# Performance work log

Hardware: AMD Instinct MI355X
Metric: run time of the kernel (lower is better)

## Reference

```python
import jax, jax.numpy as jnp
from jax import lax
import numpy as np

W_SSIM = 0.5
W_SMOOTH = 0.1
W_LR = 1.0
C1 = 0.01 ** 2
C2 = 0.03 ** 2


def avg3(x):
    # 3x3 stride-1 VALID average pool (matches F.avg_pool2d(x, 3, 1))
    return lax.reduce_window(x, 0.0, lax.add, (1, 1, 3, 3), (1, 1, 1, 1), 'VALID') / 9.0


def resize_ac(img, oh, ow):
    # bilinear resize with align_corners=True, separable gathers
    B, C, H, W = img.shape
    ys = jnp.linspace(0.0, H - 1.0, oh)
    xs = jnp.linspace(0.0, W - 1.0, ow)
    y0 = jnp.floor(ys).astype(jnp.int32); y1 = jnp.minimum(y0 + 1, H - 1); wy = ys - y0
    x0 = jnp.floor(xs).astype(jnp.int32); x1 = jnp.minimum(x0 + 1, W - 1); wx = xs - x0
    r = img[:, :, y0, :] * (1.0 - wy)[None, None, :, None] + img[:, :, y1, :] * wy[None, None, :, None]
    return r[:, :, :, x0] * (1.0 - wx) + r[:, :, :, x1] * wx


def warp_h(img, disp, sign):
    # horizontal bilinear warp: sample img at x + sign*disp (disp in units of image width),
    # align_corners=True pixel mapping, zeros padding outside the image.
    B, C, H, W = img.shape
    xb = jnp.linspace(0.0, 1.0, W)
    px = (xb[None, None, :] + sign * disp[:, 0, :, :]) * (W - 1)  # [B,H,W] pixel coords
    x0 = jnp.floor(px); f = px - x0
    x0i = x0.astype(jnp.int32); x1i = x0i + 1
    v0 = ((x0i >= 0) & (x0i < W)).astype(img.dtype)
    v1 = ((x1i >= 0) & (x1i < W)).astype(img.dtype)
    i0 = jnp.broadcast_to(jnp.clip(x0i, 0, W - 1)[:, None], (B, C, H, W))
    i1 = jnp.broadcast_to(jnp.clip(x1i, 0, W - 1)[:, None], (B, C, H, W))
    g0 = jnp.take_along_axis(img, i0, axis=3)
    g1 = jnp.take_along_axis(img, i1, axis=3)
    return g0 * (v0 * (1.0 - f))[:, None] + g1 * (v1 * f)[:, None]


def ssim(x, y):
    mu_x = avg3(x); mu_y = avg3(y)
    sig_x = avg3(x * x) - mu_x ** 2
    sig_y = avg3(y * y) - mu_y ** 2
    sig_xy = avg3(x * y) - mu_x * mu_y
    s = ((2 * mu_x * mu_y + C1) * (2 * sig_xy + C2)) / ((mu_x ** 2 + mu_y ** 2 + C1) * (sig_x + sig_y + C2))
    return jnp.clip((1.0 - s) / 2.0, 0.0, 1.0)


def smoothness(disp, img):
    dgx = disp[:, :, :, :-1] - disp[:, :, :, 1:]
    dgy = disp[:, :, :-1, :] - disp[:, :, 1:, :]
    igx = img[:, :, :, :-1] - img[:, :, :, 1:]
    igy = img[:, :, :-1, :] - img[:, :, 1:, :]
    wx = jnp.exp(-jnp.mean(jnp.abs(igx), axis=1, keepdims=True))
    wy = jnp.exp(-jnp.mean(jnp.abs(igy), axis=1, keepdims=True))
    return jnp.mean(jnp.abs(dgx * wx)) + jnp.mean(jnp.abs(dgy * wy))


def compute_loss(disps, left, right):
    B, _, H, W = left.shape
    img_loss = 0.0
    lr_loss = 0.0
    sm_loss = 0.0
    for i, d in enumerate(disps):
        r = 2 ** i
        h, w = H // r, W // r
        lpy = left if i == 0 else resize_ac(left, h, w)
        rpy = right if i == 0 else resize_ac(right, h, w)
        dl = d[:, 0:1]; dr = d[:, 1:2]
        left_est = warp_h(rpy, dl, -1.0)
        right_est = warp_h(lpy, dr, 1.0)
        rl_disp = warp_h(dr, dl, -1.0)
        lr_disp = warp_h(dl, dr, 1.0)
        l1_l = jnp.mean(jnp.abs(left_est - lpy))
        l1_r = jnp.mean(jnp.abs(right_est - rpy))
        ss_l = jnp.mean(ssim(left_est, lpy))
        ss_r = jnp.mean(ssim(right_est, rpy))
        img_loss = img_loss + W_SSIM * ss_l + (1 - W_SSIM) * l1_l + W_SSIM * ss_r + (1 - W_SSIM) * l1_r
        lr_loss = lr_loss + jnp.mean(jnp.abs(rl_disp - dl)) + jnp.mean(jnp.abs(lr_disp - dr))
        sm_loss = sm_loss + (smoothness(dl, lpy) + smoothness(dr, rpy)) / r
    return img_loss + W_SMOOTH * sm_loss + W_LR * lr_loss


def setup_inputs() -> dict:
    key = jax.random.key(0)
    ks = jax.random.split(key, 6)
    B, H, W = 16, 384, 768
    inp = {}
    for i in range(4):
        r = 2 ** i
        # disparities in units of image width; scaled to realistic ~[0, 0.1]
        inp[f'disp{i}'] = jax.random.uniform(ks[i], (B, 2, H // r, W // r), dtype=jnp.float32) * 0.1
    inp['left_image'] = jax.random.uniform(ks[4], (B, 3, H, W), dtype=jnp.float32)
    inp['right_image'] = jax.random.uniform(ks[5], (B, 3, H, W), dtype=jnp.float32)
    return inp


def reference(disp0, disp1, disp2, disp3, left_image, right_image):
    return compute_loss([disp0, disp1, disp2, disp3], left_image, right_image)
```

## Files before the change

kernel.cpp:

```cpp
#include <hip/hip_runtime.h>
#include <math.h>

#define C1F 1.0e-4f
#define C2F 9.0e-4f
#define TX 32
#define TY 8


struct ScaleArgs {
    const float* disp;
    const float* lp;
    const float* rp;
    int h, w, nx, ny, blk0, accoff;
};

__device__ __forceinline__ float2 f2(float v) { return make_float2(v, v); }
__device__ __forceinline__ float2 f2abs(float2 a) {
    return make_float2(fabsf(a.x), fabsf(a.y));
}

__device__ __forceinline__ void warp_coeffs(float px, int W, int& i0, int& i1,
                                            float& w0, float& w1) {
    float x0f = floorf(px);
    float f = px - x0f;
    int x0i = (int)x0f;
    int x1i = x0i + 1;
    float v0 = (x0i >= 0 && x0i < W) ? 1.f : 0.f;
    float v1 = (x1i >= 0 && x1i < W) ? 1.f : 0.f;
    i0 = min(max(x0i, 0), W - 1);
    i1 = min(max(x1i, 0), W - 1);
    w0 = v0 * (1.f - f);
    w1 = v1 * f;
}

template<int N>
__device__ __forceinline__ void block_acc(const float* vals, float* gacc) {
    __shared__ float sacc[N];
    if (threadIdx.x < N) sacc[threadIdx.x] = 0.f;
    __syncthreads();
#pragma unroll
    for (int k = 0; k < N; ++k) {
        float v = vals[k];
#pragma unroll
        for (int off = 32; off > 0; off >>= 1) v += __shfl_down(v, off, 64);
        if ((threadIdx.x & 63) == 0) atomicAdd(&sacc[k], v);
    }
    __syncthreads();
    if (threadIdx.x < N) atomicAdd(&gacc[threadIdx.x], sacc[threadIdx.x]);
}

__global__ void k_zero(float* acc) {
    if (threadIdx.x < 64) acc[threadIdx.x] = 0.f;
}

__device__ __forceinline__ void fused_tile(const ScaleArgs& sa, int t,
                                           float* __restrict__ accbase) {
    __shared__ float4 simg[3][(TY + 2) * (TX + 2)];
    __shared__ float2 sdisp[(TY + 2) * (TX + 2)];

    const int h = sa.h, w = sa.w;
    float* acc = accbase + sa.accoff;

    const int tileX = t % sa.nx;
    int t2 = t / sa.nx;
    const int tileY = t2 % sa.ny;
    const int b = t2 / sa.ny;

    const int xo0 = tileX * TX;
    const int yo0 = tileY * TY;
    const int tid = threadIdx.x;
    const float Wm1 = (float)(w - 1);
    const float invWm1 = 1.f / Wm1;
    const int chs = h * w;

    const float* __restrict__ dl_base = sa.disp + (b * 2 + 0) * chs;
    const float* __restrict__ dr_base = sa.disp + (b * 2 + 1) * chs;
    const float* __restrict__ limg = sa.lp + b * 3 * chs;
    const float* __restrict__ rimg = sa.rp + b * 3 * chs;

    const int NS = (TY + 2) * (TX + 2);
    const int nk = (tid + 256 < NS) ? 2 : 1;
    int xs[2], ys[2];
    float dlv[2], drv[2];
#pragma unroll
    for (int k = 0; k < 2; ++k) {
        if (k < nk) {
            int i = tid + k * 256;
            int sx = i % (TX + 2);
            int sy = i / (TX + 2);
            int x = min(max(xo0 - 1 + sx, 0), w - 1);
            int y = min(max(yo0 - 1 + sy, 0), h - 1);
            xs[k] = x; ys[k] = y;
            int off = y * w + x;
            dlv[k] = dl_base[off];
            drv[k] = dr_base[off];
        }
    }
    int i0L[2], i1L[2], i0R[2], i1R[2];
    float w0L[2], w1L[2], w0R[2], w1R[2];
    float lvv[2][3], rvv[2][3], gr0[2][3], gr1[2][3], gl0[2][3], gl1[2][3];
#pragma unroll
    for (int k = 0; k < 2; ++k) {
        if (k < nk) {
            float xb = (float)xs[k] * invWm1;
            warp_coeffs((xb - dlv[k]) * Wm1, w, i0L[k], i1L[k], w0L[k], w1L[k]);
            warp_coeffs((xb + drv[k]) * Wm1, w, i0R[k], i1R[k], w0R[k], w1R[k]);
            int rowoff = ys[k] * w;
#pragma unroll
            for (int c = 0; c < 3; ++c) {
                int co = c * chs + rowoff;
                lvv[k][c] = limg[co + xs[k]];
                rvv[k][c] = rimg[co + xs[k]];
                gr0[k][c] = rimg[co + i0L[k]];
                gr1[k][c] = rimg[co + i1L[k]];
                gl0[k][c] = limg[co + i0R[k]];
                gl1[k][c] = limg[co + i1R[k]];
            }
        }
    }
#pragma unroll
    for (int k = 0; k < 2; ++k) {
        if (k < nk) {
            int i = tid + k * 256;
            sdisp[i] = make_float2(dlv[k], drv[k]);
#pragma unroll
            for (int c = 0; c < 3; ++c) {
                float le = gr0[k][c] * w0L[k] + gr1[k][c] * w1L[k];
                float re = gl0[k][c] * w0R[k] + gl1[k][c] * w1R[k];
                simg[c][i] = make_float4(le, re, lvv[k][c], rvv[k][c]);
            }
        }
    }
    __syncthreads();

    float sums[8] = {0.f, 0.f, 0.f, 0.f, 0.f, 0.f, 0.f, 0.f};
    const int tx = tid % TX, ty = tid / TX;
    const int x = xo0 + tx, y = yo0 + ty;
    if (x < w && y < h) {
        const int s = (ty + 1) * (TX + 2) + (tx + 1);
        float2 dd = sdisp[s];
        float dl = dd.x, dr = dd.y;
#pragma unroll
        for (int c = 0; c < 3; ++c) {
            float4 v = simg[c][s];
            float2 d = f2abs(make_float2(v.x, v.y) - make_float2(v.z, v.w));
            sums[0] += d.x;
            sums[1] += d.y;
        }
        {
            float xb = (float)x * invWm1;
            int i0, i1; float w0, w1;
            warp_coeffs((xb - dl) * Wm1, w, i0, i1, w0, w1);
            const float* dr_row = dr_base + y * w;
            float rl = dr_row[i0] * w0 + dr_row[i1] * w1;
            sums[2] += fabsf(rl - dl);
            warp_coeffs((xb + dr) * Wm1, w, i0, i1, w0, w1);
            const float* dl_row = dl_base + y * w;
            float lr = dl_row[i0] * w0 + dl_row[i1] * w1;
            sums[3] += fabsf(lr - dr);
        }
        const float third = 1.f / 3.f;
        if (x < w - 1) {
            float2 d1 = sdisp[s + 1];
            float2 alr = f2(0.f);
#pragma unroll
            for (int c = 0; c < 3; ++c) {
                float4 v = simg[c][s];
                float4 v1 = simg[c][s + 1];
                alr = alr + f2abs(make_float2(v.z, v.w) - make_float2(v1.z, v1.w));
            }
            sums[4] += fabsf((dl - d1.x) * __expf(-alr.x * third)) +
                       fabsf((dr - d1.y) * __expf(-alr.y * third));
        }
        if (y < h - 1) {
            float2 d1 = sdisp[s + (TX + 2)];
            float2 alr = f2(0.f);
#pragma unroll
            for (int c = 0; c < 3; ++c) {
                float4 v = simg[c][s];
                float4 v1 = simg[c][s + (TX + 2)];
                alr = alr + f2abs(make_float2(v.z, v.w) - make_float2(v1.z, v1.w));
            }
            sums[5] += fabsf((dl - d1.x) * __expf(-alr.x * third)) +
                       fabsf((dr - d1.y) * __expf(-alr.y * third));
        }
        if (x >= 1 && x <= w - 2 && y >= 1 && y <= h - 2) {
            const float2 inv9 = f2(1.f / 9.f);
            const float2 c1 = f2(C1F), c2 = f2(C2F);
            const float2 two = f2(2.f), one = f2(1.f), half_ = f2(0.5f);
#pragma unroll 1
            for (int c = 0; c < 3; ++c) {
                float2 sX = f2(0.f), sY = f2(0.f);
                float2 sXX = f2(0.f), sYY = f2(0.f), sXY = f2(0.f);
#pragma unroll
                for (int dy = 0; dy < 3; ++dy) {
#pragma unroll
                    for (int dx = 0; dx < 3; ++dx) {
                        float4 v = simg[c][(ty + dy) * (TX + 2) + (tx + dx)];
                        float2 a = make_float2(v.x, v.y);
                        float2 bb = make_float2(v.z, v.w);
                        sX = sX + a;
                        sY = sY + bb;
                        sXX = sXX + a * a;
                        sYY = sYY + bb * bb;
                        sXY = sXY + a * bb;
                    }
                }
                float2 mx = sX * inv9, my = sY * inv9;
                float2 vx = sXX * inv9 - mx * mx;
                float2 vy = sYY * inv9 - my * my;
                float2 vxy = sXY * inv9 - mx * my;
                float2 num = (two * mx * my + c1) * (two * vxy + c2);
                float2 den = (mx * mx + my * my + c1) * (vx + vy + c2);
                float2 ss = make_float2(num.x * __builtin_amdgcn_rcpf(den.x),
                                        num.y * __builtin_amdgcn_rcpf(den.y));
                float2 v = (one - ss) * half_;
                sums[6] += fminf(fmaxf(v.x, 0.f), 1.f);
                sums[7] += fminf(fmaxf(v.y, 0.f), 1.f);
            }
        }
    }
    block_acc<8>(sums, acc);
}

__global__ void __launch_bounds__(256, 4)
k_fused0_resize(ScaleArgs s0, float* __restrict__ accbase,
                const float* __restrict__ left, const float* __restrict__ right,
                float* __restrict__ lo1, float* __restrict__ ro1,
                float* __restrict__ lo2, float* __restrict__ ro2,
                float* __restrict__ lo3, float* __restrict__ ro3,
                int B, int H, int W,
                int nFusedBlocks, long long n1, long long n2, long long n3) {
    if ((int)blockIdx.x < nFusedBlocks) {
        fused_tile(s0, blockIdx.x, accbase);
        return;
    }
    long long idx = (long long)(blockIdx.x - nFusedBlocks) * blockDim.x + threadIdx.x;
    int oh, ow;
    float* lo;
    float* ro;
    if (idx < n1) {
        oh = H / 2; ow = W / 2; lo = lo1; ro = ro1;
    } else if (idx < n1 + n2) {
        idx -= n1; oh = H / 4; ow = W / 4; lo = lo2; ro = ro2;
    } else if (idx < n1 + n2 + n3) {
        idx -= n1 + n2; oh = H / 8; ow = W / 8; lo = lo3; ro = ro3;
    } else {
        return;
    }
    long long half = (long long)B * 3 * oh * ow;
    const float* src = left;
    float* dst = lo;
    if (idx >= half) { src = right; dst = ro; idx -= half; }
    int x = (int)(idx % ow);
    long long t = idx / ow;
    int y = (int)(t % oh);
    t /= oh;
    int c = (int)(t % 3);
    int b = (int)(t / 3);
    float sy = (float)(H - 1) / (float)(oh - 1);
    float sx = (float)(W - 1) / (float)(ow - 1);
    float fy = y * sy;
    float fx = x * sx;
    int y0 = (int)floorf(fy); float wy = fy - (float)y0;
    int x0 = (int)floorf(fx); float wx = fx - (float)x0;
    int y1 = min(y0 + 1, H - 1); y0 = min(y0, H - 1);
    int x1 = min(x0 + 1, W - 1); x0 = min(x0, W - 1);
    const float* p = src + ((long long)b * 3 + c) * H * W;
    float a00 = p[(long long)y0 * W + x0];
    float a10 = p[(long long)y1 * W + x0];
    float a01 = p[(long long)y0 * W + x1];
    float a11 = p[(long long)y1 * W + x1];
    float r0 = a00 * (1.f - wy) + a10 * wy;
    float r1 = a01 * (1.f - wy) + a11 * wy;
    dst[(((long long)b * 3 + c) * oh + y) * ow + x] = r0 * (1.f - wx) + r1 * wx;
}

__global__ void __launch_bounds__(256, 4)
k_fused_small(ScaleArgs s1, ScaleArgs s2, ScaleArgs s3,
              float* __restrict__ accbase) {
    ScaleArgs sa;
    {
        int blk = blockIdx.x;
        if (blk >= s3.blk0)      sa = s3;
        else if (blk >= s2.blk0) sa = s2;
        else                     sa = s1;
    }
    fused_tile(sa, blockIdx.x - sa.blk0, accbase);
}

__global__ void k_final(const float* __restrict__ acc, float* __restrict__ out,
                        int B, int H, int W) {
    if (threadIdx.x != 0 || blockIdx.x != 0) return;
    float img = 0.f, lr = 0.f, sm = 0.f;
    for (int i = 0; i < 4; ++i) {
        int r = 1 << i;
        int h = H / r, w = W / r;
        const float* a = acc + i * 8;
        float Nl1 = (float)B * 3.f * (float)h * (float)w;
        float Nss = (float)B * 3.f * (float)(h - 2) * (float)(w - 2);
        float Nlr = (float)B * (float)h * (float)w;
        float Nsx = (float)B * (float)h * (float)(w - 1);
        float Nsy = (float)B * (float)(h - 1) * (float)w;
        img += 0.5f * (a[6] / Nss) + 0.5f * (a[0] / Nl1)
             + 0.5f * (a[7] / Nss) + 0.5f * (a[1] / Nl1);
        lr += a[2] / Nlr + a[3] / Nlr;
        sm += (a[4] / Nsx + a[5] / Nsy) / (float)r;
    }
    out[0] = img + 0.1f * sm + 1.0f * lr;
}

extern "C" void kernel_launch(void* const* d_in, const int* in_sizes, int n_in,
                              void* d_out, int out_size, void* d_ws, size_t ws_size,
                              hipStream_t stream) {
    const int B = 16, H = 384, W = 768;
    const float* disp[4] = {(const float*)d_in[0], (const float*)d_in[1],
                            (const float*)d_in[2], (const float*)d_in[3]};
    const float* left = (const float*)d_in[4];
    const float* right = (const float*)d_in[5];
    float* out = (float*)d_out;

    float* acc = (float*)d_ws;
    float* pyr = acc + 256;
    long long sz1 = (long long)B * 3 * (H / 2) * (W / 2);
    long long sz2 = (long long)B * 3 * (H / 4) * (W / 4);
    long long sz3 = (long long)B * 3 * (H / 8) * (W / 8);
    float* lp1 = pyr;
    float* rp1 = lp1 + sz1;
    float* lp2 = rp1 + sz1;
    float* rp2 = lp2 + sz2;
    float* lp3 = rp2 + sz2;
    float* rp3 = lp3 + sz3;

    const int TB = 256;
    const float* lp[4] = {left, lp1, lp2, lp3};
    const float* rp[4] = {right, rp1, rp2, rp3};
    ScaleArgs sa[4];
    for (int i = 0; i < 4; ++i) {
        int r = 1 << i;
        int h = H / r, w = W / r;
        sa[i].disp = disp[i];
        sa[i].lp = lp[i];
        sa[i].rp = rp[i];
        sa[i].h = h;
        sa[i].w = w;
        sa[i].nx = w / TX;
        sa[i].ny = h / TY;
        sa[i].accoff = i * 8;
        sa[i].blk0 = 0;
    }

    hipLaunchKernelGGL(k_zero, dim3(1), dim3(64), 0, stream, acc);

    {
        int nFused = sa[0].nx * sa[0].ny * B;
        long long n1 = 2 * sz1, n2 = 2 * sz2, n3 = 2 * sz3;
        long long nrElem = n1 + n2 + n3;
        int nResize = (int)((nrElem + TB - 1) / TB);
        hipLaunchKernelGGL(k_fused0_resize, dim3((unsigned)(nFused + nResize)), dim3(TB), 0, stream,
                           sa[0], acc, left, right, lp1, rp1, lp2, rp2, lp3, rp3,
                           B, H, W, nFused, n1, n2, n3);
    }

    {
        int b1 = sa[1].nx * sa[1].ny * B;
        int b2 = sa[2].nx * sa[2].ny * B;
        int b3 = sa[3].nx * sa[3].ny * B;
        sa[1].blk0 = 0;
        sa[2].blk0 = b1;
        sa[3].blk0 = b1 + b2;
        hipLaunchKernelGGL(k_fused_small, dim3((unsigned)(b1 + b2 + b3)), dim3(TB), 0, stream,
                           sa[1], sa[2], sa[3], acc);
    }
    hipLaunchKernelGGL(k_final, dim3(1), dim3(64), 0, stream, acc, out, B, H, W);
}
```

Before: 505.4 us.

## Fuse pyramid resize into small-scale tiles and merge all scales into one kernel

Removes the materialized image pyramid. Each small-scale tile now computes the bilinear-resized pixels, including the warped gathers, on the fly from the full-resolution images. All four scales run in a single launch, with XCD-aware block swizzling and a last-block ticket counter that does the final reduction in place of a separate kernel. This saves the pyramid write and read-back plus two launches, at the cost of more arithmetic and scattered full-resolution gathers in the small-scale tiles.

```diff
diff --git a/kernel.cpp b/kernel.cpp
--- a/kernel.cpp
+++ b/kernel.cpp
@@ -5,13 +5,16 @@
 #define C2F 9.0e-4f
 #define TX 32
 #define TY 8
+#define NSTAGE ((TY + 2) * (TX + 2))
 
 
 struct ScaleArgs {
     const float* disp;
     const float* lp;
     const float* rp;
-    int h, w, nx, ny, blk0, accoff;
+    int h, w, nx, ny, blk0, accoff, ntiles;
+    int Wf, Hf;
+    float syf, sxf;
 };
 
 __device__ __forceinline__ float2 f2(float v) { return make_float2(v, v); }
@@ -49,15 +52,22 @@
     if (threadIdx.x < N) atomicAdd(&gacc[threadIdx.x], sacc[threadIdx.x]);
 }
 
+__device__ __forceinline__ int xcd_swz(int orig, int n) {
+    int q = n >> 3, r = n & 7;
+    int x = orig & 7;
+    int base = (x < r) ? x * (q + 1) : r * (q + 1) + (x - r) * q;
+    return base + (orig >> 3);
+}
+
 __global__ void k_zero(float* acc) {
-    if (threadIdx.x < 64) acc[threadIdx.x] = 0.f;
-}
-
+    acc[threadIdx.x] = 0.f;
+}
+
+template<bool RS>
 __device__ __forceinline__ void fused_tile(const ScaleArgs& sa, int t,
-                                           float* __restrict__ accbase) {
-    __shared__ float4 simg[3][(TY + 2) * (TX + 2)];
-    __shared__ float2 sdisp[(TY + 2) * (TX + 2)];
-
+                                           float* __restrict__ accbase,
+                                           float4 (*__restrict__ simg)[NSTAGE],
+                                           float2* __restrict__ sdisp) {
     const int h = sa.h, w = sa.w;
     float* acc = accbase + sa.accoff;
 
@@ -75,59 +85,120 @@
 
     const float* __restrict__ dl_base = sa.disp + (b * 2 + 0) * chs;
     const float* __restrict__ dr_base = sa.disp + (b * 2 + 1) * chs;
-    const float* __restrict__ limg = sa.lp + b * 3 * chs;
-    const float* __restrict__ rimg = sa.rp + b * 3 * chs;
-
-    const int NS = (TY + 2) * (TX + 2);
-    const int nk = (tid + 256 < NS) ? 2 : 1;
-    int xs[2], ys[2];
-    float dlv[2], drv[2];
-#pragma unroll
-    for (int k = 0; k < 2; ++k) {
-        if (k < nk) {
-            int i = tid + k * 256;
+
+    const int nk = (tid + 256 < NSTAGE) ? 2 : 1;
+
+    if (!RS) {
+        const float* __restrict__ limg = sa.lp + b * 3 * chs;
+        const float* __restrict__ rimg = sa.rp + b * 3 * chs;
+        int xs[2], ys[2];
+        float dlv[2], drv[2];
+#pragma unroll
+        for (int k = 0; k < 2; ++k) {
+            if (k < nk) {
+                int i = tid + k * 256;
+                int sx = i % (TX + 2);
+                int sy = i / (TX + 2);
+                int x = min(max(xo0 - 1 + sx, 0), w - 1);
+                int y = min(max(yo0 - 1 + sy, 0), h - 1);
+                xs[k] = x; ys[k] = y;
+                int off = y * w + x;
+                dlv[k] = dl_base[off];
+                drv[k] = dr_base[off];
+            }
+        }
+        int i0L[2], i1L[2], i0R[2], i1R[2];
+        float w0L[2], w1L[2], w0R[2], w1R[2];
+        float lvv[2][3], rvv[2][3], gr0[2][3], gr1[2][3], gl0[2][3], gl1[2][3];
+#pragma unroll
+        for (int k = 0; k < 2; ++k) {
+            if (k < nk) {
+                float xb = (float)xs[k] * invWm1;
+                warp_coeffs((xb - dlv[k]) * Wm1, w, i0L[k], i1L[k], w0L[k], w1L[k]);
+                warp_coeffs((xb + drv[k]) * Wm1, w, i0R[k], i1R[k], w0R[k], w1R[k]);
+                int rowoff = ys[k] * w;
+#pragma unroll
+                for (int c = 0; c < 3; ++c) {
+                    int co = c * chs + rowoff;
+                    lvv[k][c] = limg[co + xs[k]];
+                    rvv[k][c] = rimg[co + xs[k]];
+                    gr0[k][c] = rimg[co + i0L[k]];
+                    gr1[k][c] = rimg[co + i1L[k]];
+                    gl0[k][c] = limg[co + i0R[k]];
+                    gl1[k][c] = limg[co + i1R[k]];
+                }
+            }
+        }
+#pragma unroll
+        for (int k = 0; k < 2; ++k) {
+            if (k < nk) {
+                int i = tid + k * 256;
+                sdisp[i] = make_float2(dlv[k], drv[k]);
+#pragma unroll
+                for (int c = 0; c < 3; ++c) {
+                    float le = gr0[k][c] * w0L[k] + gr1[k][c] * w1L[k];
+                    float re = gl0[k][c] * w0R[k] + gl1[k][c] * w1R[k];
+                    simg[c][i] = make_float4(le, re, lvv[k][c], rvv[k][c]);
+                }
+            }
+        }
+    } else {
+        const int Wf = sa.Wf;
+        const int chsF = sa.Hf * Wf;
+        const float* __restrict__ limgF = sa.lp + b * 3 * chsF;
+        const float* __restrict__ rimgF = sa.rp + b * 3 * chsF;
+        for (int k = 0; k < nk; ++k) {
+            int i = tid + (k << 8);
             int sx = i % (TX + 2);
             int sy = i / (TX + 2);
             int x = min(max(xo0 - 1 + sx, 0), w - 1);
             int y = min(max(yo0 - 1 + sy, 0), h - 1);
-            xs[k] = x; ys[k] = y;
             int off = y * w + x;
-            dlv[k] = dl_base[off];
-            drv[k] = dr_base[off];
-        }
-    }
-    int i0L[2], i1L[2], i0R[2], i1R[2];
-    float w0L[2], w1L[2], w0R[2], w1R[2];
-    float lvv[2][3], rvv[2][3], gr0[2][3], gr1[2][3], gl0[2][3], gl1[2][3];
-#pragma unroll
-    for (int k = 0; k < 2; ++k) {
-        if (k < nk) {
-            float xb = (float)xs[k] * invWm1;
-            warp_coeffs((xb - dlv[k]) * Wm1, w, i0L[k], i1L[k], w0L[k], w1L[k]);
-            warp_coeffs((xb + drv[k]) * Wm1, w, i0R[k], i1R[k], w0R[k], w1R[k]);
-            int rowoff = ys[k] * w;
+            float dlv = dl_base[off];
+            float drv = dr_base[off];
+            float fy = (float)y * sa.syf;
+            int y0 = (int)floorf(fy);
+            float wy = fy - (float)y0;
+            int y1 = min(y0 + 1, sa.Hf - 1);
+            y0 = min(y0, sa.Hf - 1);
+            float omwy = 1.f - wy;
+            int ro0 = y0 * Wf, ro1 = y1 * Wf;
+            float xb = (float)x * invWm1;
+            int i0L, i1L, i0R, i1R;
+            float w0L, w1L, w0R, w1R;
+            warp_coeffs((xb - dlv) * Wm1, w, i0L, i1L, w0L, w1L);
+            warp_coeffs((xb + drv) * Wm1, w, i0R, i1R, w0R, w1R);
+            int px_[5] = {x, i0L, i1L, i0R, i1R};
+            int x0p[5], x1p[5];
+            float wxp[5];
+#pragma unroll
+            for (int p = 0; p < 5; ++p) {
+                float fx = (float)px_[p] * sa.sxf;
+                int x0 = (int)floorf(fx);
+                wxp[p] = fx - (float)x0;
+                x1p[p] = min(x0 + 1, Wf - 1);
+                x0p[p] = min(x0, Wf - 1);
+            }
+            auto BIL = [&](const float* P0, const float* P1, int p) -> float {
+                float r0 = P0[x0p[p]] * omwy + P1[x0p[p]] * wy;
+                float r1 = P0[x1p[p]] * omwy + P1[x1p[p]] * wy;
+                return r0 * (1.f - wxp[p]) + r1 * wxp[p];
+            };
+            sdisp[i] = make_float2(dlv, drv);
 #pragma unroll
             for (int c = 0; c < 3; ++c) {
-                int co = c * chs + rowoff;
-                lvv[k][c] = limg[co + xs[k]];
-                rvv[k][c] = rimg[co + xs[k]];
-                gr0[k][c] = rimg[co + i0L[k]];
-                gr1[k][c] = rimg[co + i1L[k]];
-                gl0[k][c] = limg[co + i0R[k]];
-                gl1[k][c] = limg[co + i1R[k]];
-            }
-        }
-    }
-#pragma unroll
-    for (int k = 0; k < 2; ++k) {
-        if (k < nk) {
-            int i = tid + k * 256;
-            sdisp[i] = make_float2(dlv[k], drv[k]);
-#pragma unroll
-            for (int c = 0; c < 3; ++c) {
-                float le = gr0[k][c] * w0L[k] + gr1[k][c] * w1L[k];
-                float re = gl0[k][c] * w0R[k] + gl1[k][c] * w1R[k];
-                simg[c][i] = make_float4(le, re, lvv[k][c], rvv[k][c]);
+                const float* L0 = limgF + c * chsF + ro0;
+                const float* L1 = limgF + c * chsF + ro1;
+                const float* R0 = rimgF + c * chsF + ro0;
+                const float* R1 = rimgF + c * chsF + ro1;
+                float lv = BIL(L0, L1, 0);
+                float rv = BIL(R0, R1, 0);
+                float g0 = BIL(R0, R1, 1);
+                float g1 = BIL(R0, R1, 2);
+                float h0 = BIL(L0, L1, 3);
+                float h1 = BIL(L0, L1, 4);
+                simg[c][i] = make_float4(g0 * w0L + g1 * w1L,
+                                         h0 * w0R + h1 * w1R, lv, rv);
             }
         }
     }
@@ -224,90 +295,53 @@
 }
 
 __global__ void __launch_bounds__(256, 4)
-k_fused0_resize(ScaleArgs s0, float* __restrict__ accbase,
-                const float* __restrict__ left, const float* __restrict__ right,
-                float* __restrict__ lo1, float* __restrict__ ro1,
-                float* __restrict__ lo2, float* __restrict__ ro2,
-                float* __restrict__ lo3, float* __restrict__ ro3,
-                int B, int H, int W,
-                int nFusedBlocks, long long n1, long long n2, long long n3) {
-    if ((int)blockIdx.x < nFusedBlocks) {
-        fused_tile(s0, blockIdx.x, accbase);
-        return;
-    }
-    long long idx = (long long)(blockIdx.x - nFusedBlocks) * blockDim.x + threadIdx.x;
-    int oh, ow;
-    float* lo;
-    float* ro;
-    if (idx < n1) {
-        oh = H / 2; ow = W / 2; lo = lo1; ro = ro1;
-    } else if (idx < n1 + n2) {
-        idx -= n1; oh = H / 4; ow = W / 4; lo = lo2; ro = ro2;
-    } else if (idx < n1 + n2 + n3) {
-        idx -= n1 + n2; oh = H / 8; ow = W / 8; lo = lo3; ro = ro3;
+k_main(ScaleArgs s0, ScaleArgs s1, ScaleArgs s2, ScaleArgs s3,
+       float* __restrict__ accbase, float* __restrict__ out,
+       int nTotal, int B, int H, int W) {
+    __shared__ float4 simg[3][NSTAGE];
+    __shared__ float2 sdisp[NSTAGE];
+
+    int blk = blockIdx.x;
+    if (blk < s1.blk0) {
+        int t = xcd_swz(blk, s0.ntiles);
+        fused_tile<false>(s0, t, accbase, simg, sdisp);
     } else {
-        return;
-    }
-    long long half = (long long)B * 3 * oh * ow;
-    const float* src = left;
-    float* dst = lo;
-    if (idx >= half) { src = right; dst = ro; idx -= half; }
-    int x = (int)(idx % ow);
-    long long t = idx / ow;
-    int y = (int)(t % oh);
-    t /= oh;
-    int c = (int)(t % 3);
-    int b = (int)(t / 3);
-    float sy = (float)(H - 1) / (float)(oh - 1);
-    float sx = (float)(W - 1) / (float)(ow - 1);
-    float fy = y * sy;
-    float fx = x * sx;
-    int y0 = (int)floorf(fy); float wy = fy - (float)y0;
-    int x0 = (int)floorf(fx); float wx = fx - (float)x0;
-    int y1 = min(y0 + 1, H - 1); y0 = min(y0, H - 1);
-    int x1 = min(x0 + 1, W - 1); x0 = min(x0, W - 1);
-    const float* p = src + ((long long)b * 3 + c) * H * W;
-    float a00 = p[(long long)y0 * W + x0];
-    float a10 = p[(long long)y1 * W + x0];
-    float a01 = p[(long long)y0 * W + x1];
-    float a11 = p[(long long)y1 * W + x1];
-    float r0 = a00 * (1.f - wy) + a10 * wy;
-    float r1 = a01 * (1.f - wy) + a11 * wy;
-    dst[(((long long)b * 3 + c) * oh + y) * ow + x] = r0 * (1.f - wx) + r1 * wx;
-}
-
-__global__ void __launch_bounds__(256, 4)
-k_fused_small(ScaleArgs s1, ScaleArgs s2, ScaleArgs s3,
-              float* __restrict__ accbase) {
-    ScaleArgs sa;
-    {
-        int blk = blockIdx.x;
-        if (blk >= s3.blk0)      sa = s3;
-        else if (blk >= s2.blk0) sa = s2;
-        else                     sa = s1;
-    }
-    fused_tile(sa, blockIdx.x - sa.blk0, accbase);
-}
-
-__global__ void k_final(const float* __restrict__ acc, float* __restrict__ out,
-                        int B, int H, int W) {
-    if (threadIdx.x != 0 || blockIdx.x != 0) return;
-    float img = 0.f, lr = 0.f, sm = 0.f;
-    for (int i = 0; i < 4; ++i) {
-        int r = 1 << i;
-        int h = H / r, w = W / r;
-        const float* a = acc + i * 8;
-        float Nl1 = (float)B * 3.f * (float)h * (float)w;
-        float Nss = (float)B * 3.f * (float)(h - 2) * (float)(w - 2);
-        float Nlr = (float)B * (float)h * (float)w;
-        float Nsx = (float)B * (float)h * (float)(w - 1);
-        float Nsy = (float)B * (float)(h - 1) * (float)w;
-        img += 0.5f * (a[6] / Nss) + 0.5f * (a[0] / Nl1)
-             + 0.5f * (a[7] / Nss) + 0.5f * (a[1] / Nl1);
-        lr += a[2] / Nlr + a[3] / Nlr;
-        sm += (a[4] / Nsx + a[5] / Nsy) / (float)r;
-    }
-    out[0] = img + 0.1f * sm + 1.0f * lr;
+        ScaleArgs sa = (blk >= s3.blk0) ? s3 : ((blk >= s2.blk0) ? s2 : s1);
+        int t = xcd_swz(blk - sa.blk0, sa.ntiles);
+        fused_tile<true>(sa, t, accbase, simg, sdisp);
+    }
+
+    __syncthreads();
+    if (threadIdx.x == 0) {
+        __threadfence();
+        unsigned* tic = (unsigned*)(accbase + 64);
+        unsigned prev = __hip_atomic_fetch_add(tic, 1u, __ATOMIC_ACQ_REL,
+                                               __HIP_MEMORY_SCOPE_AGENT);
+        if (prev == (unsigned)(nTotal - 1)) {
+            float a[32];
+#pragma unroll 1
+            for (int k = 0; k < 32; ++k)
+                a[k] = __hip_atomic_load(&accbase[k], __ATOMIC_RELAXED,
+                                         __HIP_MEMORY_SCOPE_AGENT);
+            float img = 0.f, lr = 0.f, sm = 0.f;
+#pragma unroll 1
+            for (int i = 0; i < 4; ++i) {
+                int r = 1 << i;
+                int h = H / r, w = W / r;
+                const float* ac = a + i * 8;
+                float Nl1 = (float)B * 3.f * (float)h * (float)w;
+                float Nss = (float)B * 3.f * (float)(h - 2) * (float)(w - 2);
+                float Nlr = (float)B * (float)h * (float)w;
+                float Nsx = (float)B * (float)h * (float)(w - 1);
+                float Nsy = (float)B * (float)(h - 1) * (float)w;
+                img += 0.5f * (ac[6] / Nss) + 0.5f * (ac[0] / Nl1)
+                     + 0.5f * (ac[7] / Nss) + 0.5f * (ac[1] / Nl1);
+                lr += ac[2] / Nlr + ac[3] / Nlr;
+                sm += (ac[4] / Nsx + ac[5] / Nsy) / (float)r;
+            }
+            out[0] = img + 0.1f * sm + 1.0f * lr;
+        }
+    }
 }
 
 extern "C" void kernel_launch(void* const* d_in, const int* in_sizes, int n_in,
@@ -319,58 +353,32 @@
     const float* left = (const float*)d_in[4];
     const float* right = (const float*)d_in[5];
     float* out = (float*)d_out;
-
     float* acc = (float*)d_ws;
-    float* pyr = acc + 256;
-    long long sz1 = (long long)B * 3 * (H / 2) * (W / 2);
-    long long sz2 = (long long)B * 3 * (H / 4) * (W / 4);
-    long long sz3 = (long long)B * 3 * (H / 8) * (W / 8);
-    float* lp1 = pyr;
-    float* rp1 = lp1 + sz1;
-    float* lp2 = rp1 + sz1;
-    float* rp2 = lp2 + sz2;
-    float* lp3 = rp2 + sz2;
-    float* rp3 = lp3 + sz3;
-
-    const int TB = 256;
-    const float* lp[4] = {left, lp1, lp2, lp3};
-    const float* rp[4] = {right, rp1, rp2, rp3};
+
     ScaleArgs sa[4];
+    int blk0 = 0;
     for (int i = 0; i < 4; ++i) {
         int r = 1 << i;
         int h = H / r, w = W / r;
         sa[i].disp = disp[i];
-        sa[i].lp = lp[i];
-        sa[i].rp = rp[i];
+        sa[i].lp = left;
+        sa[i].rp = right;
         sa[i].h = h;
         sa[i].w = w;
         sa[i].nx = w / TX;
         sa[i].ny = h / TY;
         sa[i].accoff = i * 8;
-        sa[i].blk0 = 0;
-    }
-
-    hipLaunchKernelGGL(k_zero, dim3(1), dim3(64), 0, stream, acc);
-
-    {
-        int nFused = sa[0].nx * sa[0].ny * B;
-        long long n1 = 2 * sz1, n2 = 2 * sz2, n3 = 2 * sz3;
-        long long nrElem = n1 + n2 + n3;
-        int nResize = (int)((nrElem + TB - 1) / TB);
-        hipLaunchKernelGGL(k_fused0_resize, dim3((unsigned)(nFused + nResize)), dim3(TB), 0, stream,
-                           sa[0], acc, left, right, lp1, rp1, lp2, rp2, lp3, rp3,
-                           B, H, W, nFused, n1, n2, n3);
-    }
-
-    {
-        int b1 = sa[1].nx * sa[1].ny * B;
-        int b2 = sa[2].nx * sa[2].ny * B;
-        int b3 = sa[3].nx * sa[3].ny * B;
-        sa[1].blk0 = 0;
-        sa[2].blk0 = b1;
-        sa[3].blk0 = b1 + b2;
-        hipLaunchKernelGGL(k_fused_small, dim3((unsigned)(b1 + b2 + b3)), dim3(TB), 0, stream,
-                           sa[1], sa[2], sa[3], acc);
-    }
-    hipLaunchKernelGGL(k_final, dim3(1), dim3(64), 0, stream, acc, out, B, H, W);
-}
+        sa[i].ntiles = sa[i].nx * sa[i].ny * B;
+        sa[i].blk0 = blk0;
+        blk0 += sa[i].ntiles;
+        sa[i].Wf = W;
+        sa[i].Hf = H;
+        sa[i].syf = (i == 0) ? 1.f : (float)(H - 1) / (float)(h - 1);
+        sa[i].sxf = (i == 0) ? 1.f : (float)(W - 1) / (float)(w - 1);
+    }
+    int nTotal = blk0;
+
+    hipLaunchKernelGGL(k_zero, dim3(1), dim3(128), 0, stream, acc);
+    hipLaunchKernelGGL(k_main, dim3((unsigned)nTotal), dim3(256), 0, stream,
+                       sa[0], sa[1], sa[2], sa[3], acc, out, nTotal, B, H, W);
+}
```

Result: slower. 1.798 ms (+255.8%).

## Stage disparity-windowed image rows in LDS for warp gathers, reshape tiles

Applied to the files above, without the earlier changes.

Each tile now loads full row segments of the left/right images and disparities into shared memory. The segments are widened by a per-scale maximum-disparity margin, so the bilinear warp gathers and the left-right consistency lookups read from LDS instead of doing scattered global loads. A per-block check falls back to global gathers when any disparity is outside the assumed range, so results stay correct. The tile becomes 64x4 and blocks get an XCD-aware swizzle. LDS use per block goes up, which lowers occupancy (the fused0 launch bound drops to 3), and each tile stages a wider halo than it strictly needs.

```diff
diff --git a/kernel.cpp b/kernel.cpp
--- a/kernel.cpp
+++ b/kernel.cpp
@@ -3,15 +3,19 @@
 
 #define C1F 1.0e-4f
 #define C2F 9.0e-4f
-#define TX 32
-#define TY 8
+#define TX 64
+#define TY 4
+#define NROWS (TY + 2)
+#define NSTAGE ((TY + 2) * (TX + 2))
 
 
 struct ScaleArgs {
     const float* disp;
     const float* lp;
     const float* rp;
-    int h, w, nx, ny, blk0, accoff;
+    int h, w, nx, ny, blk0, accoff, ntiles;
+    int maxd;
+    float dmax;
 };
 
 __device__ __forceinline__ float2 f2(float v) { return make_float2(v, v); }
@@ -49,15 +53,25 @@
     if (threadIdx.x < N) atomicAdd(&gacc[threadIdx.x], sacc[threadIdx.x]);
 }
 
+__device__ __forceinline__ int xcd_swz(int orig, int n) {
+    int q = n >> 3, r = n & 7;
+    int x = orig & 7;
+    int base = (x < r) ? x * (q + 1) : r * (q + 1) + (x - r) * q;
+    return base + (orig >> 3);
+}
+
 __global__ void k_zero(float* acc) {
     if (threadIdx.x < 64) acc[threadIdx.x] = 0.f;
 }
 
-__device__ __forceinline__ void fused_tile(const ScaleArgs& sa, int t,
-                                           float* __restrict__ accbase) {
-    __shared__ float4 simg[3][(TY + 2) * (TX + 2)];
-    __shared__ float2 sdisp[(TY + 2) * (TX + 2)];
-
+template<int SW>
+__device__ void fused_tile(const ScaleArgs& sa, int t, float* __restrict__ accbase,
+                           float4* __restrict__ simg,
+                           float* __restrict__ sLp,
+                           float* __restrict__ sRp,
+                           float* __restrict__ sdl,
+                           float* __restrict__ sdr,
+                           int* __restrict__ sok) {
     const int h = sa.h, w = sa.w;
     float* acc = accbase + sa.accoff;
 
@@ -72,62 +86,88 @@
     const float Wm1 = (float)(w - 1);
     const float invWm1 = 1.f / Wm1;
     const int chs = h * w;
+    const int MAXD = sa.maxd;
+    const int lx0 = xo0 - 1;
+    const int rx0 = xo0 - 1 - MAXD;
+    const int gy0 = yo0 - 1;
 
     const float* __restrict__ dl_base = sa.disp + (b * 2 + 0) * chs;
     const float* __restrict__ dr_base = sa.disp + (b * 2 + 1) * chs;
     const float* __restrict__ limg = sa.lp + b * 3 * chs;
     const float* __restrict__ rimg = sa.rp + b * 3 * chs;
 
-    const int NS = (TY + 2) * (TX + 2);
-    const int nk = (tid + 256 < NS) ? 2 : 1;
-    int xs[2], ys[2];
-    float dlv[2], drv[2];
-#pragma unroll
-    for (int k = 0; k < 2; ++k) {
-        if (k < nk) {
-            int i = tid + k * 256;
-            int sx = i % (TX + 2);
-            int sy = i / (TX + 2);
-            int x = min(max(xo0 - 1 + sx, 0), w - 1);
-            int y = min(max(yo0 - 1 + sy, 0), h - 1);
-            xs[k] = x; ys[k] = y;
-            int off = y * w + x;
-            dlv[k] = dl_base[off];
-            drv[k] = dr_base[off];
-        }
-    }
-    int i0L[2], i1L[2], i0R[2], i1R[2];
-    float w0L[2], w1L[2], w0R[2], w1R[2];
-    float lvv[2][3], rvv[2][3], gr0[2][3], gr1[2][3], gl0[2][3], gl1[2][3];
-#pragma unroll
-    for (int k = 0; k < 2; ++k) {
-        if (k < nk) {
-            float xb = (float)xs[k] * invWm1;
-            warp_coeffs((xb - dlv[k]) * Wm1, w, i0L[k], i1L[k], w0L[k], w1L[k]);
-            warp_coeffs((xb + drv[k]) * Wm1, w, i0R[k], i1R[k], w0R[k], w1R[k]);
-            int rowoff = ys[k] * w;
+    if (tid == 0) *sok = 1;
+    __syncthreads();
+
+    for (int i = tid; i < 6 * NROWS * SW; i += 256) {
+        int k = i % SW;
+        int tt = i / SW;
+        int r = tt % NROWS;
+        int cc = tt / NROWS;
+        int y = min(max(gy0 + r, 0), h - 1);
+        if (cc < 3) {
+            int x = min(max(lx0 + k, 0), w - 1);
+            sLp[(cc * NROWS + r) * SW + k] = limg[cc * chs + y * w + x];
+        } else {
+            int c = cc - 3;
+            int x = min(max(rx0 + k, 0), w - 1);
+            sRp[(c * NROWS + r) * SW + k] = rimg[c * chs + y * w + x];
+        }
+    }
+    bool bad = false;
+    for (int i = tid; i < 2 * NROWS * SW; i += 256) {
+        int k = i % SW;
+        int tt = i / SW;
+        int r = tt % NROWS;
+        int y = min(max(gy0 + r, 0), h - 1);
+        float v;
+        if (tt < NROWS) {
+            int x = min(max(lx0 + k, 0), w - 1);
+            v = dl_base[y * w + x];
+            sdl[r * SW + k] = v;
+        } else {
+            int x = min(max(rx0 + k, 0), w - 1);
+            v = dr_base[y * w + x];
+            sdr[r * SW + k] = v;
+        }
+        bad = bad || !(v >= 0.f && v <= sa.dmax);
+    }
+    if (bad) *sok = 0;
+    __syncthreads();
+    const bool ok = (*sok != 0);
+
+    for (int i = tid; i < NSTAGE; i += 256) {
+        int sx = i % (TX + 2);
+        int sy = i / (TX + 2);
+        int x = min(max(xo0 - 1 + sx, 0), w - 1);
+        float dl = sdl[sy * SW + (x - lx0)];
+        float dr = sdr[sy * SW + (x - rx0)];
+        float xb = (float)x * invWm1;
+        int i0L, i1L, i0R, i1R;
+        float w0L, w1L, w0R, w1R;
+        warp_coeffs((xb - dl) * Wm1, w, i0L, i1L, w0L, w1L);
+        warp_coeffs((xb + dr) * Wm1, w, i0R, i1R, w0R, w1R);
+        if (ok) {
+            int a0 = i0L - rx0, a1 = i1L - rx0;
+            int b0 = i0R - lx0, b1 = i1R - lx0;
+            int xl = x - lx0, xr = x - rx0;
+#pragma unroll
+            for (int c = 0; c < 3; ++c) {
+                const float* R = sRp + (c * NROWS + sy) * SW;
+                const float* L = sLp + (c * NROWS + sy) * SW;
+                float le = R[a0] * w0L + R[a1] * w1L;
+                float re = L[b0] * w0R + L[b1] * w1R;
+                simg[c * NSTAGE + i] = make_float4(le, re, L[xl], R[xr]);
+            }
+        } else {
+            int y = min(max(gy0 + sy, 0), h - 1);
+            int rowoff = y * w;
 #pragma unroll
             for (int c = 0; c < 3; ++c) {
                 int co = c * chs + rowoff;
-                lvv[k][c] = limg[co + xs[k]];
-                rvv[k][c] = rimg[co + xs[k]];
-                gr0[k][c] = rimg[co + i0L[k]];
-                gr1[k][c] = rimg[co + i1L[k]];
-                gl0[k][c] = limg[co + i0R[k]];
-                gl1[k][c] = limg[co + i1R[k]];
-            }
-        }
-    }
-#pragma unroll
-    for (int k = 0; k < 2; ++k) {
-        if (k < nk) {
-            int i = tid + k * 256;
-            sdisp[i] = make_float2(dlv[k], drv[k]);
-#pragma unroll
-            for (int c = 0; c < 3; ++c) {
-                float le = gr0[k][c] * w0L[k] + gr1[k][c] * w1L[k];
-                float re = gl0[k][c] * w0R[k] + gl1[k][c] * w1R[k];
-                simg[c][i] = make_float4(le, re, lvv[k][c], rvv[k][c]);
+                float le = rimg[co + i0L] * w0L + rimg[co + i1L] * w1L;
+                float re = limg[co + i0R] * w0R + limg[co + i1R] * w1R;
+                simg[c * NSTAGE + i] = make_float4(le, re, limg[co + x], rimg[co + x]);
             }
         }
     }
@@ -138,11 +178,13 @@
     const int x = xo0 + tx, y = yo0 + ty;
     if (x < w && y < h) {
         const int s = (ty + 1) * (TX + 2) + (tx + 1);
-        float2 dd = sdisp[s];
-        float dl = dd.x, dr = dd.y;
+        const int kdl = (ty + 1) * SW + (tx + 1);
+        const int kdr = kdl + MAXD;
+        float dl = sdl[kdl];
+        float dr = sdr[kdr];
 #pragma unroll
         for (int c = 0; c < 3; ++c) {
-            float4 v = simg[c][s];
+            float4 v = simg[c * NSTAGE + s];
             float2 d = f2abs(make_float2(v.x, v.y) - make_float2(v.z, v.w));
             sums[0] += d.x;
             sums[1] += d.y;
@@ -151,38 +193,50 @@
             float xb = (float)x * invWm1;
             int i0, i1; float w0, w1;
             warp_coeffs((xb - dl) * Wm1, w, i0, i1, w0, w1);
-            const float* dr_row = dr_base + y * w;
-            float rl = dr_row[i0] * w0 + dr_row[i1] * w1;
+            float rl;
+            if (ok) {
+                rl = sdr[(ty + 1) * SW + (i0 - rx0)] * w0 +
+                     sdr[(ty + 1) * SW + (i1 - rx0)] * w1;
+            } else {
+                const float* drr = dr_base + y * w;
+                rl = drr[i0] * w0 + drr[i1] * w1;
+            }
             sums[2] += fabsf(rl - dl);
             warp_coeffs((xb + dr) * Wm1, w, i0, i1, w0, w1);
-            const float* dl_row = dl_base + y * w;
-            float lr = dl_row[i0] * w0 + dl_row[i1] * w1;
+            float lr;
+            if (ok) {
+                lr = sdl[(ty + 1) * SW + (i0 - lx0)] * w0 +
+                     sdl[(ty + 1) * SW + (i1 - lx0)] * w1;
+            } else {
+                const float* dlr = dl_base + y * w;
+                lr = dlr[i0] * w0 + dlr[i1] * w1;
+            }
             sums[3] += fabsf(lr - dr);
         }
         const float third = 1.f / 3.f;
         if (x < w - 1) {
-            float2 d1 = sdisp[s + 1];
+            float dlx = sdl[kdl + 1], drx = sdr[kdr + 1];
             float2 alr = f2(0.f);
 #pragma unroll
             for (int c = 0; c < 3; ++c) {
-                float4 v = simg[c][s];
-                float4 v1 = simg[c][s + 1];
+                float4 v = simg[c * NSTAGE + s];
+                float4 v1 = simg[c * NSTAGE + s + 1];
                 alr = alr + f2abs(make_float2(v.z, v.w) - make_float2(v1.z, v1.w));
             }
-            sums[4] += fabsf((dl - d1.x) * __expf(-alr.x * third)) +
-                       fabsf((dr - d1.y) * __expf(-alr.y * third));
+            sums[4] += fabsf((dl - dlx) * __expf(-alr.x * third)) +
+                       fabsf((dr - drx) * __expf(-alr.y * third));
         }
         if (y < h - 1) {
-            float2 d1 = sdisp[s + (TX + 2)];
+            float dly = sdl[kdl + SW], dry = sdr[kdr + SW];
             float2 alr = f2(0.f);
 #pragma unroll
             for (int c = 0; c < 3; ++c) {
-                float4 v = simg[c][s];
-                float4 v1 = simg[c][s + (TX + 2)];
+                float4 v = simg[c * NSTAGE + s];
+                float4 v1 = simg[c * NSTAGE + s + (TX + 2)];
                 alr = alr + f2abs(make_float2(v.z, v.w) - make_float2(v1.z, v1.w));
             }
-            sums[5] += fabsf((dl - d1.x) * __expf(-alr.x * third)) +
-                       fabsf((dr - d1.y) * __expf(-alr.y * third));
+            sums[5] += fabsf((dl - dly) * __expf(-alr.x * third)) +
+                       fabsf((dr - dry) * __expf(-alr.y * third));
         }
         if (x >= 1 && x <= w - 2 && y >= 1 && y <= h - 2) {
             const float2 inv9 = f2(1.f / 9.f);
@@ -196,7 +250,7 @@
                 for (int dy = 0; dy < 3; ++dy) {
 #pragma unroll
                     for (int dx = 0; dx < 3; ++dx) {
-                        float4 v = simg[c][(ty + dy) * (TX + 2) + (tx + dx)];
+                        float4 v = simg[c * NSTAGE + (ty + dy) * (TX + 2) + (tx + dx)];
                         float2 a = make_float2(v.x, v.y);
                         float2 bb = make_float2(v.z, v.w);
                         sX = sX + a;
@@ -223,7 +277,10 @@
     block_acc<8>(sums, acc);
 }
 
-__global__ void __launch_bounds__(256, 4)
+#define SW0 144
+#define SWB 106
+
+__global__ void __launch_bounds__(256, 3)
 k_fused0_resize(ScaleArgs s0, float* __restrict__ accbase,
                 const float* __restrict__ left, const float* __restrict__ right,
                 float* __restrict__ lo1, float* __restrict__ ro1,
@@ -231,8 +288,16 @@
                 float* __restrict__ lo3, float* __restrict__ ro3,
                 int B, int H, int W,
                 int nFusedBlocks, long long n1, long long n2, long long n3) {
+    __shared__ float4 simg[3 * NSTAGE];
+    __shared__ float sL[3 * NROWS * SW0];
+    __shared__ float sR[3 * NROWS * SW0];
+    __shared__ float sdl[NROWS * SW0];
+    __shared__ float sdr[NROWS * SW0];
+    __shared__ int sok;
+
     if ((int)blockIdx.x < nFusedBlocks) {
-        fused_tile(s0, blockIdx.x, accbase);
+        int t = xcd_swz((int)blockIdx.x, nFusedBlocks);
+        fused_tile<SW0>(s0, t, accbase, simg, sL, sR, sdl, sdr, &sok);
         return;
     }
     long long idx = (long long)(blockIdx.x - nFusedBlocks) * blockDim.x + threadIdx.x;
@@ -279,14 +344,22 @@
 __global__ void __launch_bounds__(256, 4)
 k_fused_small(ScaleArgs s1, ScaleArgs s2, ScaleArgs s3,
               float* __restrict__ accbase) {
+    __shared__ float4 simg[3 * NSTAGE];
+    __shared__ float sL[3 * NROWS * SWB];
+    __shared__ float sR[3 * NROWS * SWB];
+    __shared__ float sdl[NROWS * SWB];
+    __shared__ float sdr[NROWS * SWB];
+    __shared__ int sok;
+
     ScaleArgs sa;
     {
-        int blk = blockIdx.x;
+        int blk = (int)blockIdx.x;
         if (blk >= s3.blk0)      sa = s3;
         else if (blk >= s2.blk0) sa = s2;
         else                     sa = s1;
     }
-    fused_tile(sa, blockIdx.x - sa.blk0, accbase);
+    int t = xcd_swz((int)blockIdx.x - sa.blk0, sa.ntiles);
+    fused_tile<SWB>(sa, t, accbase, simg, sL, sR, sdl, sdr, &sok);
 }
 
 __global__ void k_final(const float* __restrict__ acc, float* __restrict__ out,
@@ -335,6 +408,7 @@
     const int TB = 256;
     const float* lp[4] = {left, lp1, lp2, lp3};
     const float* rp[4] = {right, rp1, rp2, rp3};
+    const int maxd_tab[4] = {77, 39, 20, 10};
     ScaleArgs sa[4];
     for (int i = 0; i < 4; ++i) {
         int r = 1 << i;
@@ -344,16 +418,19 @@
         sa[i].rp = rp[i];
         sa[i].h = h;
         sa[i].w = w;
-        sa[i].nx = w / TX;
-        sa[i].ny = h / TY;
+        sa[i].nx = (w + TX - 1) / TX;
+        sa[i].ny = (h + TY - 1) / TY;
         sa[i].accoff = i * 8;
+        sa[i].ntiles = sa[i].nx * sa[i].ny * B;
         sa[i].blk0 = 0;
+        sa[i].maxd = maxd_tab[i];
+        sa[i].dmax = (float)maxd_tab[i] / (float)(w - 1);
     }
 
     hipLaunchKernelGGL(k_zero, dim3(1), dim3(64), 0, stream, acc);
 
     {
-        int nFused = sa[0].nx * sa[0].ny * B;
+        int nFused = sa[0].ntiles;
         long long n1 = 2 * sz1, n2 = 2 * sz2, n3 = 2 * sz3;
         long long nrElem = n1 + n2 + n3;
         int nResize = (int)((nrElem + TB - 1) / TB);
@@ -363,9 +440,9 @@
     }
 
     {
-        int b1 = sa[1].nx * sa[1].ny * B;
-        int b2 = sa[2].nx * sa[2].ny * B;
-        int b3 = sa[3].nx * sa[3].ny * B;
+        int b1 = sa[1].ntiles;
+        int b2 = sa[2].ntiles;
+        int b3 = sa[3].ntiles;
         sa[1].blk0 = 0;
         sa[2].blk0 = b1;
         sa[3].blk0 = b1 + b2;
```

New measurement: 732.2 us. 1.45x slower.
